# Kernel optimization log

Measured on AMD Instinct MI355X. Metric: run time of the kernel, lower is better.

Reference implementation:

```python
import jax, jax.numpy as jnp
import numpy as np

DIM = 768
HEADS = 12
HEAD_DIM = DIM // HEADS
SCALE = float(HEAD_DIM) ** 0.5  # original multiplies by sqrt(head_dim) (qk_scale=None)


def setup_inputs() -> dict:
    key = jax.random.key(0)
    ks = jax.random.split(key, 6)
    B, N, C = 4, 2048, DIM
    x = jax.random.normal(ks[0], (B, N, C), dtype=jnp.float32)
    qkv_w = jax.random.normal(ks[1], (3 * C, C), dtype=jnp.float32) * (C ** -0.5)
    proj_w = jax.random.normal(ks[2], (C, C), dtype=jnp.float32) * (C ** -0.5)
    proj_b = jnp.zeros((C,), dtype=jnp.float32)
    ln_gamma = jnp.ones((C,), dtype=jnp.float32)
    ln_beta = jnp.zeros((C,), dtype=jnp.float32)
    return {"x": x, "qkv_w": qkv_w, "proj_w": proj_w, "proj_b": proj_b,
            "ln_gamma": ln_gamma, "ln_beta": ln_beta}


def reference(x, qkv_w, proj_w, proj_b, ln_gamma, ln_beta):
    B, N, C = x.shape
    H, D = HEADS, HEAD_DIM
    # qkv: Linear(dim, 3*dim, bias=False) -> reshape (B,N,3,H,D) -> permute to (3,B,H,N,D)
    qkv = jnp.einsum('bnc,oc->bno', x, qkv_w).reshape(B, N, 3, H, D)
    qkv = jnp.transpose(qkv, (2, 0, 3, 1, 4))  # [3,B,H,N,D]
    q, k, v = qkv[0], qkv[1], qkv[2]
    # explicit N x N attention (faithful to the hand-coded matmul path)
    attn = jnp.einsum('bhnd,bhmd->bhnm', q, k) * SCALE
    attn = jax.nn.softmax(attn, axis=-1)
    # dropout is identity at inference
    x1 = jnp.einsum('bhnm,bhmd->bhnd', attn, v)
    x1 = jnp.transpose(x1, (0, 2, 1, 3)).reshape(B, N, C)
    x1 = jnp.einsum('bnc,oc->bno', x1, proj_w) + proj_b
    out = x + x1
    # LayerNorm over last dim (eps = 1e-5, torch default)
    mu = jnp.mean(out, axis=-1, keepdims=True)
    var = jnp.var(out, axis=-1, keepdims=True)
    out = (out - mu) * jax.lax.rsqrt(var + 1e-5) * ln_gamma + ln_beta
    return out
```

## Files before the change

kernel.cpp:

```cpp
#include <hip/hip_runtime.h>

typedef unsigned short u16;
typedef __attribute__((ext_vector_type(8))) short bf16x8;
typedef __attribute__((ext_vector_type(8))) _Float16 f16x8;
typedef __attribute__((ext_vector_type(4))) float f32x4;
typedef __attribute__((ext_vector_type(4))) unsigned short us4;
typedef __attribute__((ext_vector_type(4))) unsigned int u32x4;

#define DEV static __device__ __forceinline__

DEV u16 bf_rne(float x){
    unsigned int u = __builtin_bit_cast(unsigned int, x);
    return (u16)((u + 0x7fffu + ((u >> 16) & 1u)) >> 16);
}
DEV u16 f16_rne(float x){ _Float16 h = (_Float16)x; return __builtin_bit_cast(unsigned short, h); }
DEV unsigned int cvtpk_bf16(float a, float b){
    unsigned int r;
    asm("v_cvt_pk_bf16_f32 %0, %1, %2" : "=v"(r) : "v"(a), "v"(b));
    return r;
}
DEV float exp2_fast(float x){
    float r;
    asm("v_exp_f32 %0, %1" : "=v"(r) : "v"(x));
    return r;
}
DEV void gload_lds16(const void* g, void* l){
    __builtin_amdgcn_global_load_lds((const __attribute__((address_space(1))) unsigned int*)g,
                                     (__attribute__((address_space(3))) unsigned int*)l, 16, 0, 0);
}

#define QSCALE 11.541560327111707f
#define DEFER_THR 11.0f

#define SW(r,cb) ((((cb) ^ ((r)&7)))*8)

__global__ __launch_bounds__(256) void k_prep(const float4* __restrict__ x, const float4* __restrict__ w,
                                              const float4* __restrict__ pw,
                                              u16* __restrict__ xh, u16* __restrict__ xl,
                                              u16* __restrict__ wf, u16* __restrict__ pwh){
    int i = blockIdx.x*256 + threadIdx.x;
    if (i < 1572864){
        float4 v = x[i];
        float vv[4] = {v.x, v.y, v.z, v.w};
        us4 h, l;
        #pragma unroll
        for (int j = 0; j < 4; ++j){
            _Float16 hh = (_Float16)vv[j];
            h[j] = __builtin_bit_cast(unsigned short, hh);
            _Float16 ll = (_Float16)(vv[j] - (float)hh);
            l[j] = __builtin_bit_cast(unsigned short, ll);
        }
        ((us4*)xh)[i] = h;
        ((us4*)xl)[i] = l;
    } else if (i < 1572864 + 442368){
        int j = i - 1572864;
        float4 v = w[j];
        us4 h = { f16_rne(v.x), f16_rne(v.y), f16_rne(v.z), f16_rne(v.w) };
        ((us4*)wf)[j] = h;
    } else {
        int j = i - 2015232;
        float4 v = pw[j];
        us4 h = { bf_rne(v.x), bf_rne(v.y), bf_rne(v.z), bf_rne(v.w) };
        ((us4*)pwh)[j] = h;
    }
}

__global__ __launch_bounds__(256, 3) void k_qkv(const u16* __restrict__ xh_, const u16* __restrict__ xl_,
                                                const u16* __restrict__ wf_,
                                                u16* __restrict__ qf, u16* __restrict__ kf,
                                                u16* __restrict__ vt){
    __shared__ u16 Ah[128*64], Al[128*64], Bf[128*64];
    const int tid = threadIdx.x, lane = tid & 63, wid = tid >> 6;
    const int lm = lane & 15, lg = lane >> 4;
    const int n0 = blockIdx.x * 128, m0 = blockIdx.y * 128;
    const int t = n0 / 768;
    const bool is_v = (t == 2);
    const int wm = (wid >> 1) * 64, wn = (wid & 1) * 64;
    f32x4 acc[4][4];
    const f32x4 z = {0.f, 0.f, 0.f, 0.f};
    #pragma unroll
    for (int i = 0; i < 4; ++i) for (int j = 0; j < 4; ++j) acc[i][j] = z;

    const int c0 = tid;
    for (int kp = 0; kp < 12; ++kp){
        const int kb = kp * 64;
        #pragma unroll
        for (int i = 0; i < 4; ++i){
            int c = c0 + i*256;
            int r = c >> 3, j = c & 7;
            int sj = (j ^ (r & 7)) * 8;
            gload_lds16(xh_ + (size_t)(m0+r)*768 + kb + sj, Ah + c*8);
            if (!is_v)
                gload_lds16(xl_ + (size_t)(m0+r)*768 + kb + sj, Al + c*8);
            gload_lds16(wf_ + (size_t)(n0+r)*768 + kb + sj, Bf + c*8);
        }
        __syncthreads();
        #pragma unroll
        for (int ks = 0; ks < 2; ++ks){
            f16x8 a_h[4], a_l[4], b_f[4];
            #pragma unroll
            for (int mt = 0; mt < 4; ++mt){
                int r = wm + mt*16 + lm, cb = lg + 4*ks;
                a_h[mt] = *(const f16x8*)(Ah + r*64 + SW(r,cb));
                if (!is_v) a_l[mt] = *(const f16x8*)(Al + r*64 + SW(r,cb));
            }
            #pragma unroll
            for (int nt = 0; nt < 4; ++nt){
                int r = wn + nt*16 + lm, cb = lg + 4*ks;
                b_f[nt] = *(const f16x8*)(Bf + r*64 + SW(r,cb));
            }
            #pragma unroll
            for (int mt = 0; mt < 4; ++mt)
            #pragma unroll
            for (int nt = 0; nt < 4; ++nt){
                acc[mt][nt] = __builtin_amdgcn_mfma_f32_16x16x32_f16(a_h[mt], b_f[nt], acc[mt][nt], 0,0,0);
                if (!is_v)
                    acc[mt][nt] = __builtin_amdgcn_mfma_f32_16x16x32_f16(a_l[mt], b_f[nt], acc[mt][nt], 0,0,0);
            }
        }
        __syncthreads();
    }
    const int nb = n0 % 768;
    #pragma unroll
    for (int mt = 0; mt < 4; ++mt)
    #pragma unroll
    for (int nt = 0; nt < 4; ++nt)
    #pragma unroll
    for (int rr = 0; rr < 4; ++rr){
        int grow = m0 + wm + mt*16 + lg*4 + rr;
        int dcol = wn + nt*16 + lm;
        int b = grow >> 11, n = grow & 2047;
        int head = (nb + dcol) >> 6;
        int d    = (nb + dcol) & 63;
        float v = acc[mt][nt][rr];
        if (t == 0)      qf[((size_t)((b*12 + head)*2048 + n))*64 + d] = f16_rne(v * QSCALE);
        else if (t == 1) kf[((size_t)((b*12 + head)*2048 + n))*64 + d] = f16_rne(v);
        else             vt[((size_t)((b*12 + head)*64 + d))*2048 + n] = bf_rne(v);
    }
}

__global__ __launch_bounds__(256) void k_attn(const u16* __restrict__ qf, const u16* __restrict__ kf,
                                              const u16* __restrict__ vt, u16* __restrict__ x1h){
    __shared__ u16 Kf[2][64*64], Vs[2][64*64];
    const int tid = threadIdx.x, lane = tid & 63, wid = tid >> 6;
    const int lm = lane & 15, lg = lane >> 4;
    const size_t bh_base = (size_t)blockIdx.y * 2048 * 64;
    const int q0 = blockIdx.x * 64;

    f16x8 qb[2];
    {
        const u16* qp = qf + bh_base + (size_t)(q0 + wid*16 + lm)*64;
        qb[0] = *(const f16x8*)(qp + lg*8);
        qb[1] = *(const f16x8*)(qp + lg*8 + 32);
    }
    f32x4 o_acc[4];
    const f32x4 z = {0.f,0.f,0.f,0.f};
    #pragma unroll
    for (int i = 0; i < 4; ++i) o_acc[i] = z;
    float m_run = -INFINITY, l_run = 0.f;

    const int srcA = ((lg & 1) * 2) * 16 + lm;
    const int srcB = srcA + 16;
    const int hi_sel = lg >> 1;

    const int r0 = tid >> 3, cb0 = tid & 7;
    const int dK0 = r0*64 + SW(r0,cb0),      dK1 = (r0+32)*64 + SW(r0+32,cb0);
    const u16* kbase = kf + bh_base + r0*64 + cb0*8;
    const u16* vbase = vt + bh_base + (size_t)r0*2048 + cb0*8;

    bf16x8 sK0, sK1, sV0, sV1;
    sK0 = *(const bf16x8*)(kbase);
    sK1 = *(const bf16x8*)(kbase + 2048);
    sV0 = *(const bf16x8*)(vbase);
    sV1 = *(const bf16x8*)(vbase + 32*2048);
    *(bf16x8*)(Kf[0] + dK0) = sK0;  *(bf16x8*)(Kf[0] + dK1) = sK1;
    *(bf16x8*)(Vs[0] + dK0) = sV0;  *(bf16x8*)(Vs[0] + dK1) = sV1;
    __syncthreads();

    for (int kt = 0; kt < 32; ++kt){
        const int cur = kt & 1;
        if (kt < 31){
            const u16* kp = kbase + (kt+1)*4096;
            const u16* vp = vbase + (kt+1)*64;
            sK0 = *(const bf16x8*)(kp);
            sK1 = *(const bf16x8*)(kp + 2048);
            sV0 = *(const bf16x8*)(vp);
            sV1 = *(const bf16x8*)(vp + 32*2048);
        }
        const u16* Kc = Kf[cur];
        const u16* Vc = Vs[cur];
        f32x4 st[4];
        #pragma unroll
        for (int i = 0; i < 4; ++i) st[i] = z;
        #pragma unroll
        for (int ks = 0; ks < 2; ++ks){
            #pragma unroll
            for (int nt = 0; nt < 4; ++nt){
                int r = nt*16 + lm, cb = lg + 4*ks;
                f16x8 ka = *(const f16x8*)(Kc + r*64 + SW(r,cb));
                st[nt] = __builtin_amdgcn_mfma_f32_16x16x32_f16(ka, qb[ks], st[nt], 0,0,0);
            }
        }
        float mx0 = fmaxf(fmaxf(st[0][0], st[0][1]), fmaxf(st[0][2], st[0][3]));
        float mx1 = fmaxf(fmaxf(st[1][0], st[1][1]), fmaxf(st[1][2], st[1][3]));
        float mx2 = fmaxf(fmaxf(st[2][0], st[2][1]), fmaxf(st[2][2], st[2][3]));
        float mx3 = fmaxf(fmaxf(st[3][0], st[3][1]), fmaxf(st[3][2], st[3][3]));
        float lmax = fmaxf(fmaxf(mx0, mx1), fmaxf(mx2, mx3));
        lmax = fmaxf(lmax, __shfl_xor(lmax, 16, 64));
        lmax = fmaxf(lmax, __shfl_xor(lmax, 32, 64));
        if (__any(lmax > m_run + DEFER_THR)){
            float mnew = fmaxf(m_run, lmax);
            float corr = exp2_fast(m_run - mnew);
            m_run = mnew;
            l_run *= corr;
            #pragma unroll
            for (int rr = 0; rr < 4; ++rr){
                float cq = __shfl(corr, (lane & 48) | (lg*4 + rr), 64);
                #pragma unroll
                for (int dt = 0; dt < 4; ++dt) o_acc[dt][rr] *= cq;
            }
        }
        float p[16];
        #pragma unroll
        for (int nt = 0; nt < 4; ++nt)
        #pragma unroll
        for (int rr = 0; rr < 4; ++rr)
            p[nt*4+rr] = exp2_fast(st[nt][rr] - m_run);
        float s01 = (p[0]+p[1]) + (p[2]+p[3]);
        float s23 = (p[4]+p[5]) + (p[6]+p[7]);
        float s45 = (p[8]+p[9]) + (p[10]+p[11]);
        float s67 = (p[12]+p[13]) + (p[14]+p[15]);
        float rsum = (s01+s23) + (s45+s67);
        rsum += __shfl_xor(rsum, 16, 64);
        rsum += __shfl_xor(rsum, 32, 64);
        l_run += rsum;
        unsigned int pk[4][2];
        #pragma unroll
        for (int nt = 0; nt < 4; ++nt)
        #pragma unroll
        for (int h = 0; h < 2; ++h)
            pk[nt][h] = cvtpk_bf16(p[nt*4 + 2*h], p[nt*4 + 2*h + 1]);
        #pragma unroll
        for (int ks = 0; ks < 2; ++ks){
            unsigned int w0a = __shfl(pk[ks*2][0],   srcA, 64);
            unsigned int w0b = __shfl(pk[ks*2+1][0], srcA, 64);
            unsigned int w1a = __shfl(pk[ks*2][1],   srcA, 64);
            unsigned int w1b = __shfl(pk[ks*2+1][1], srcA, 64);
            unsigned int w2a = __shfl(pk[ks*2][0],   srcB, 64);
            unsigned int w2b = __shfl(pk[ks*2+1][0], srcB, 64);
            unsigned int w3a = __shfl(pk[ks*2][1],   srcB, 64);
            unsigned int w3b = __shfl(pk[ks*2+1][1], srcB, 64);
            u32x4 wv;
            wv[0] = hi_sel ? w0b : w0a;
            wv[1] = hi_sel ? w1b : w1a;
            wv[2] = hi_sel ? w2b : w2a;
            wv[3] = hi_sel ? w3b : w3a;
            bf16x8 pa = __builtin_bit_cast(bf16x8, wv);
            #pragma unroll
            for (int dt = 0; dt < 4; ++dt){
                int r = dt*16 + lm, cb = lg + 4*ks;
                bf16x8 vb = *(const bf16x8*)(Vc + r*64 + SW(r,cb));
                o_acc[dt] = __builtin_amdgcn_mfma_f32_16x16x32_bf16(pa, vb, o_acc[dt], 0,0,0);
            }
        }
        __syncthreads();
        if (kt < 31){
            u16* Kn = Kf[cur ^ 1];
            u16* Vn = Vs[cur ^ 1];
            *(bf16x8*)(Kn + dK0) = sK0;  *(bf16x8*)(Kn + dK1) = sK1;
            *(bf16x8*)(Vn + dK0) = sV0;  *(bf16x8*)(Vn + dK1) = sV1;
        }
        __syncthreads();
    }
    const int b = blockIdx.y / 12, hh = blockIdx.y % 12;
    #pragma unroll
    for (int rr = 0; rr < 4; ++rr){
        float lr = __shfl(l_run, (lane & 48) | (lg*4 + rr), 64);
        float linv = 1.0f / lr;
        int qrow = q0 + wid*16 + lg*4 + rr;
        #pragma unroll
        for (int dt = 0; dt < 4; ++dt){
            int cc = hh*64 + dt*16 + lm;
            x1h[((size_t)(b*2048 + qrow))*768 + cc] = bf_rne(o_acc[dt][rr] * linv);
        }
    }
}

__global__ __launch_bounds__(256) void k_proj(const u16* __restrict__ x1h, const u16* __restrict__ pwh,
                                              const float* __restrict__ pb, const float* __restrict__ xres,
                                              float* __restrict__ out){
    __shared__ u16 Ah[128*64], Bh[64*64];
    const int tid = threadIdx.x, lane = tid & 63, wid = tid >> 6;
    const int lm = lane & 15, lg = lane >> 4;
    const int n0 = blockIdx.x * 64, m0 = blockIdx.y * 128;
    const int wm = (wid >> 1) * 64, wn = (wid & 1) * 32;
    f32x4 acc[4][2];
    const f32x4 z = {0.f,0.f,0.f,0.f};
    #pragma unroll
    for (int i = 0; i < 4; ++i) for (int j = 0; j < 2; ++j) acc[i][j] = z;

    for (int kp = 0; kp < 12; ++kp){
        const int kb = kp * 64;
        #pragma unroll
        for (int c = tid; c < 1024; c += 256){
            int r = c >> 3, cb = c & 7;
            *(bf16x8*)(Ah + r*64 + SW(r,cb)) = *(const bf16x8*)(x1h + (size_t)(m0+r)*768 + kb + cb*8);
        }
        #pragma unroll
        for (int c = tid; c < 512; c += 256){
            int r = c >> 3, cb = c & 7;
            *(bf16x8*)(Bh + r*64 + SW(r,cb)) = *(const bf16x8*)(pwh + (size_t)(n0+r)*768 + kb + cb*8);
        }
        __syncthreads();
        #pragma unroll
        for (int ks = 0; ks < 2; ++ks){
            bf16x8 af[4], bfr[2];
            #pragma unroll
            for (int mt = 0; mt < 4; ++mt){
                int r = wm + mt*16 + lm, cb = lg + 4*ks;
                af[mt] = *(const bf16x8*)(Ah + r*64 + SW(r,cb));
            }
            #pragma unroll
            for (int nt = 0; nt < 2; ++nt){
                int r = wn + nt*16 + lm, cb = lg + 4*ks;
                bfr[nt] = *(const bf16x8*)(Bh + r*64 + SW(r,cb));
            }
            #pragma unroll
            for (int mt = 0; mt < 4; ++mt)
            #pragma unroll
            for (int nt = 0; nt < 2; ++nt)
                acc[mt][nt] = __builtin_amdgcn_mfma_f32_16x16x32_bf16(af[mt], bfr[nt], acc[mt][nt], 0,0,0);
        }
        __syncthreads();
    }
    #pragma unroll
    for (int mt = 0; mt < 4; ++mt)
    #pragma unroll
    for (int nt = 0; nt < 2; ++nt)
    #pragma unroll
    for (int rr = 0; rr < 4; ++rr){
        int grow = m0 + wm + mt*16 + lg*4 + rr;
        int gcol = n0 + wn + nt*16 + lm;
        size_t o = (size_t)grow*768 + gcol;
        out[o] = acc[mt][nt][rr] + pb[gcol] + xres[o];
    }
}

__global__ __launch_bounds__(256) void k_ln(float* __restrict__ out, const float* __restrict__ gamma,
                                            const float* __restrict__ beta){
    const int tid = threadIdx.x, lane = tid & 63, wid = tid >> 6;
    float* p = out + (size_t)blockIdx.x * 768;
    float v[3], s = 0.f, s2 = 0.f;
    #pragma unroll
    for (int j = 0; j < 3; ++j){ v[j] = p[tid + j*256]; s += v[j]; s2 += v[j]*v[j]; }
    #pragma unroll
    for (int mm = 1; mm < 64; mm <<= 1){ s += __shfl_xor(s, mm, 64); s2 += __shfl_xor(s2, mm, 64); }
    __shared__ float red[8];
    if (lane == 0){ red[wid] = s; red[4 + wid] = s2; }
    __syncthreads();
    s  = red[0] + red[1] + red[2] + red[3];
    s2 = red[4] + red[5] + red[6] + red[7];
    const float mu  = s * (1.0f/768.0f);
    const float var = s2 * (1.0f/768.0f) - mu*mu;
    const float inv = rsqrtf(var + 1e-5f);
    #pragma unroll
    for (int j = 0; j < 3; ++j){
        int c = tid + j*256;
        p[c] = (v[j] - mu) * inv * gamma[c] + beta[c];
    }
}

extern "C" void kernel_launch(void* const* d_in, const int* in_sizes, int n_in,
                              void* d_out, int out_size, void* d_ws, size_t ws_size,
                              hipStream_t stream){
    const float* x      = (const float*)d_in[0];
    const float* qkv_w  = (const float*)d_in[1];
    const float* proj_w = (const float*)d_in[2];
    const float* pb     = (const float*)d_in[3];
    const float* gamma  = (const float*)d_in[4];
    const float* beta   = (const float*)d_in[5];
    float* out = (float*)d_out;

    constexpr size_t SZ_X   = 8192ull * 768;
    constexpr size_t SZ_W   = 2304ull * 768;
    constexpr size_t SZ_PW  = 768ull * 768;
    constexpr size_t TOTAL  = 6*SZ_X + SZ_W + SZ_PW;
    if (ws_size < TOTAL * sizeof(u16)) return;

    u16* ws  = (u16*)d_ws;
    u16* xh  = ws;
    u16* xl  = xh  + SZ_X;
    u16* wf  = xl  + SZ_X;
    u16* pwh = wf  + SZ_W;
    u16* qf  = pwh + SZ_PW;
    u16* kf  = qf  + SZ_X;
    u16* vt  = kf  + SZ_X;
    u16* x1h = vt  + SZ_X;

    k_prep<<<8448, 256, 0, stream>>>((const float4*)x, (const float4*)qkv_w, (const float4*)proj_w,
                                     xh, xl, wf, pwh);
    k_qkv <<<dim3(18, 64), 256, 0, stream>>>(xh, xl, wf, qf, kf, vt);
    k_attn<<<dim3(32, 48), 256, 0, stream>>>(qf, kf, vt, x1h);
    k_proj<<<dim3(12, 64), 256, 0, stream>>>(x1h, pwh, pb, x, out);
    k_ln  <<<8192, 256, 0, stream>>>(out, gamma, beta);
}
```

Baseline: 330.3 us.

## Drop split-f16 x in QKV GEMM, async LDS staging and MFMA row sums in attention

The QKV GEMM stops using the hi/lo f16 split of x and does a single f16 MFMA per tile. That removes one LDS buffer and half the MFMAs, and occupancy is raised to 4 blocks. The attention kernel now stages K/V with direct global-to-LDS loads instead of register round-trips, which removes one barrier per iteration. It also computes softmax row sums with an extra MFMA against a ones vector instead of shuffle reductions, and uses v_max3 for the row max. Dropping the low part lowers the precision of Q/K, which the scaled logits may amplify.

```diff
diff --git a/kernel.cpp b/kernel.cpp
--- a/kernel.cpp
+++ b/kernel.cpp
@@ -24,6 +24,11 @@
     asm("v_exp_f32 %0, %1" : "=v"(r) : "v"(x));
     return r;
 }
+DEV float max3f(float a, float b, float c){
+    float r;
+    asm("v_max3_f32 %0, %1, %2, %3" : "=v"(r) : "v"(a), "v"(b), "v"(c));
+    return r;
+}
 DEV void gload_lds16(const void* g, void* l){
     __builtin_amdgcn_global_load_lds((const __attribute__((address_space(1))) unsigned int*)g,
                                      (__attribute__((address_space(3))) unsigned int*)l, 16, 0, 0);
@@ -36,22 +41,13 @@
 
 __global__ __launch_bounds__(256) void k_prep(const float4* __restrict__ x, const float4* __restrict__ w,
                                               const float4* __restrict__ pw,
-                                              u16* __restrict__ xh, u16* __restrict__ xl,
-                                              u16* __restrict__ wf, u16* __restrict__ pwh){
+                                              u16* __restrict__ xf, u16* __restrict__ wf,
+                                              u16* __restrict__ pwh){
     int i = blockIdx.x*256 + threadIdx.x;
     if (i < 1572864){
         float4 v = x[i];
-        float vv[4] = {v.x, v.y, v.z, v.w};
-        us4 h, l;
-        #pragma unroll
-        for (int j = 0; j < 4; ++j){
-            _Float16 hh = (_Float16)vv[j];
-            h[j] = __builtin_bit_cast(unsigned short, hh);
-            _Float16 ll = (_Float16)(vv[j] - (float)hh);
-            l[j] = __builtin_bit_cast(unsigned short, ll);
-        }
-        ((us4*)xh)[i] = h;
-        ((us4*)xl)[i] = l;
+        us4 h = { f16_rne(v.x), f16_rne(v.y), f16_rne(v.z), f16_rne(v.w) };
+        ((us4*)xf)[i] = h;
     } else if (i < 1572864 + 442368){
         int j = i - 1572864;
         float4 v = w[j];
@@ -65,44 +61,40 @@
     }
 }
 
-__global__ __launch_bounds__(256, 3) void k_qkv(const u16* __restrict__ xh_, const u16* __restrict__ xl_,
-                                                const u16* __restrict__ wf_,
+__global__ __launch_bounds__(256, 4) void k_qkv(const u16* __restrict__ xf_, const u16* __restrict__ wf_,
                                                 u16* __restrict__ qf, u16* __restrict__ kf,
                                                 u16* __restrict__ vt){
-    __shared__ u16 Ah[128*64], Al[128*64], Bf[128*64];
+    __shared__ u16 Ah[128*64], Bf[128*64];
     const int tid = threadIdx.x, lane = tid & 63, wid = tid >> 6;
     const int lm = lane & 15, lg = lane >> 4;
     const int n0 = blockIdx.x * 128, m0 = blockIdx.y * 128;
     const int t = n0 / 768;
-    const bool is_v = (t == 2);
     const int wm = (wid >> 1) * 64, wn = (wid & 1) * 64;
     f32x4 acc[4][4];
     const f32x4 z = {0.f, 0.f, 0.f, 0.f};
     #pragma unroll
     for (int i = 0; i < 4; ++i) for (int j = 0; j < 4; ++j) acc[i][j] = z;
 
-    const int c0 = tid;
+    const int rA = tid >> 3, jA = tid & 7;
+    const int sj = (jA ^ (rA & 7)) * 8;
+    const u16* asrc = xf_ + (size_t)(m0 + rA)*768 + sj;
+    const u16* bsrc = wf_ + (size_t)(n0 + rA)*768 + sj;
+
     for (int kp = 0; kp < 12; ++kp){
         const int kb = kp * 64;
         #pragma unroll
         for (int i = 0; i < 4; ++i){
-            int c = c0 + i*256;
-            int r = c >> 3, j = c & 7;
-            int sj = (j ^ (r & 7)) * 8;
-            gload_lds16(xh_ + (size_t)(m0+r)*768 + kb + sj, Ah + c*8);
-            if (!is_v)
-                gload_lds16(xl_ + (size_t)(m0+r)*768 + kb + sj, Al + c*8);
-            gload_lds16(wf_ + (size_t)(n0+r)*768 + kb + sj, Bf + c*8);
+            gload_lds16(asrc + (size_t)i*(32*768) + kb, Ah + tid*8 + i*2048);
+            gload_lds16(bsrc + (size_t)i*(32*768) + kb, Bf + tid*8 + i*2048);
         }
         __syncthreads();
         #pragma unroll
         for (int ks = 0; ks < 2; ++ks){
-            f16x8 a_h[4], a_l[4], b_f[4];
+            f16x8 a_f[4], b_f[4];
             #pragma unroll
             for (int mt = 0; mt < 4; ++mt){
                 int r = wm + mt*16 + lm, cb = lg + 4*ks;
-                a_h[mt] = *(const f16x8*)(Ah + r*64 + SW(r,cb));
-                if (!is_v) a_l[mt] = *(const f16x8*)(Al + r*64 + SW(r,cb));
+                a_f[mt] = *(const f16x8*)(Ah + r*64 + SW(r,cb));
             }
             #pragma unroll
             for (int nt = 0; nt < 4; ++nt){
@@ -112,11 +104,8 @@
             #pragma unroll
             for (int mt = 0; mt < 4; ++mt)
             #pragma unroll
-            for (int nt = 0; nt < 4; ++nt){
-                acc[mt][nt] = __builtin_amdgcn_mfma_f32_16x16x32_f16(a_h[mt], b_f[nt], acc[mt][nt], 0,0,0);
-                if (!is_v)
-                    acc[mt][nt] = __builtin_amdgcn_mfma_f32_16x16x32_f16(a_l[mt], b_f[nt], acc[mt][nt], 0,0,0);
-            }
+            for (int nt = 0; nt < 4; ++nt)
+                acc[mt][nt] = __builtin_amdgcn_mfma_f32_16x16x32_f16(a_f[mt], b_f[nt], acc[mt][nt], 0,0,0);
         }
         __syncthreads();
     }
@@ -153,40 +142,42 @@
         qb[0] = *(const f16x8*)(qp + lg*8);
         qb[1] = *(const f16x8*)(qp + lg*8 + 32);
     }
-    f32x4 o_acc[4];
+    f32x4 o_acc[4], o_sum;
     const f32x4 z = {0.f,0.f,0.f,0.f};
     #pragma unroll
     for (int i = 0; i < 4; ++i) o_acc[i] = z;
-    float m_run = -INFINITY, l_run = 0.f;
+    o_sum = z;
+    float m_run = -INFINITY;
+    bf16x8 ones;
+    #pragma unroll
+    for (int i = 0; i < 8; ++i) ones[i] = (short)16256;
 
     const int srcA = ((lg & 1) * 2) * 16 + lm;
     const int srcB = srcA + 16;
     const int hi_sel = lg >> 1;
 
-    const int r0 = tid >> 3, cb0 = tid & 7;
-    const int dK0 = r0*64 + SW(r0,cb0),      dK1 = (r0+32)*64 + SW(r0+32,cb0);
-    const u16* kbase = kf + bh_base + r0*64 + cb0*8;
-    const u16* vbase = vt + bh_base + (size_t)r0*2048 + cb0*8;
-
-    bf16x8 sK0, sK1, sV0, sV1;
-    sK0 = *(const bf16x8*)(kbase);
-    sK1 = *(const bf16x8*)(kbase + 2048);
-    sV0 = *(const bf16x8*)(vbase);
-    sV1 = *(const bf16x8*)(vbase + 32*2048);
-    *(bf16x8*)(Kf[0] + dK0) = sK0;  *(bf16x8*)(Kf[0] + dK1) = sK1;
-    *(bf16x8*)(Vs[0] + dK0) = sV0;  *(bf16x8*)(Vs[0] + dK1) = sV1;
+    const int rA = tid >> 3, jA = tid & 7;
+    const int sj = (jA ^ (rA & 7)) * 8;
+    const u16* ksrc = kf + bh_base + rA*64 + sj;
+    const u16* vsrc = vt + bh_base + (size_t)rA*2048 + sj;
+
+    #define STAGE(kt_, b_) do { \
+        const u16* kp_ = ksrc + (size_t)(kt_)*4096; \
+        const u16* vp_ = vsrc + (size_t)(kt_)*64; \
+        u16* lk_ = Kf[b_] + tid*8; \
+        u16* lv_ = Vs[b_] + tid*8; \
+        gload_lds16(kp_,            lk_); \
+        gload_lds16(kp_ + 2048,     lk_ + 2048); \
+        gload_lds16(vp_,            lv_); \
+        gload_lds16(vp_ + 32*2048,  lv_ + 2048); \
+    } while(0)
+
+    STAGE(0, 0);
     __syncthreads();
 
     for (int kt = 0; kt < 32; ++kt){
         const int cur = kt & 1;
-        if (kt < 31){
-            const u16* kp = kbase + (kt+1)*4096;
-            const u16* vp = vbase + (kt+1)*64;
-            sK0 = *(const bf16x8*)(kp);
-            sK1 = *(const bf16x8*)(kp + 2048);
-            sV0 = *(const bf16x8*)(vp);
-            sV1 = *(const bf16x8*)(vp + 32*2048);
-        }
+        if (kt < 31) STAGE(kt + 1, cur ^ 1);
         const u16* Kc = Kf[cur];
         const u16* Vc = Vs[cur];
         f32x4 st[4];
@@ -201,21 +192,22 @@
                 st[nt] = __builtin_amdgcn_mfma_f32_16x16x32_f16(ka, qb[ks], st[nt], 0,0,0);
             }
         }
-        float mx0 = fmaxf(fmaxf(st[0][0], st[0][1]), fmaxf(st[0][2], st[0][3]));
-        float mx1 = fmaxf(fmaxf(st[1][0], st[1][1]), fmaxf(st[1][2], st[1][3]));
-        float mx2 = fmaxf(fmaxf(st[2][0], st[2][1]), fmaxf(st[2][2], st[2][3]));
-        float mx3 = fmaxf(fmaxf(st[3][0], st[3][1]), fmaxf(st[3][2], st[3][3]));
-        float lmax = fmaxf(fmaxf(mx0, mx1), fmaxf(mx2, mx3));
+        float g0 = max3f(st[0][0], st[0][1], st[0][2]);
+        float g1 = max3f(st[0][3], st[1][0], st[1][1]);
+        float g2 = max3f(st[1][2], st[1][3], st[2][0]);
+        float g3 = max3f(st[2][1], st[2][2], st[2][3]);
+        float g4 = max3f(st[3][0], st[3][1], st[3][2]);
+        float lmax = fmaxf(max3f(g0, g1, g2), max3f(g3, g4, st[3][3]));
         lmax = fmaxf(lmax, __shfl_xor(lmax, 16, 64));
         lmax = fmaxf(lmax, __shfl_xor(lmax, 32, 64));
         if (__any(lmax > m_run + DEFER_THR)){
             float mnew = fmaxf(m_run, lmax);
             float corr = exp2_fast(m_run - mnew);
             m_run = mnew;
-            l_run *= corr;
             #pragma unroll
             for (int rr = 0; rr < 4; ++rr){
                 float cq = __shfl(corr, (lane & 48) | (lg*4 + rr), 64);
+                o_sum[rr] *= cq;
                 #pragma unroll
                 for (int dt = 0; dt < 4; ++dt) o_acc[dt][rr] *= cq;
             }
@@ -226,14 +218,6 @@
         #pragma unroll
         for (int rr = 0; rr < 4; ++rr)
             p[nt*4+rr] = exp2_fast(st[nt][rr] - m_run);
-        float s01 = (p[0]+p[1]) + (p[2]+p[3]);
-        float s23 = (p[4]+p[5]) + (p[6]+p[7]);
-        float s45 = (p[8]+p[9]) + (p[10]+p[11]);
-        float s67 = (p[12]+p[13]) + (p[14]+p[15]);
-        float rsum = (s01+s23) + (s45+s67);
-        rsum += __shfl_xor(rsum, 16, 64);
-        rsum += __shfl_xor(rsum, 32, 64);
-        l_run += rsum;
         unsigned int pk[4][2];
         #pragma unroll
         for (int nt = 0; nt < 4; ++nt)
@@ -256,6 +240,7 @@
             wv[2] = hi_sel ? w2b : w2a;
             wv[3] = hi_sel ? w3b : w3a;
             bf16x8 pa = __builtin_bit_cast(bf16x8, wv);
+            o_sum = __builtin_amdgcn_mfma_f32_16x16x32_bf16(pa, ones, o_sum, 0,0,0);
             #pragma unroll
             for (int dt = 0; dt < 4; ++dt){
                 int r = dt*16 + lm, cb = lg + 4*ks;
@@ -264,19 +249,12 @@
             }
         }
         __syncthreads();
-        if (kt < 31){
-            u16* Kn = Kf[cur ^ 1];
-            u16* Vn = Vs[cur ^ 1];
-            *(bf16x8*)(Kn + dK0) = sK0;  *(bf16x8*)(Kn + dK1) = sK1;
-            *(bf16x8*)(Vn + dK0) = sV0;  *(bf16x8*)(Vn + dK1) = sV1;
-        }
-        __syncthreads();
-    }
+    }
+    #undef STAGE
     const int b = blockIdx.y / 12, hh = blockIdx.y % 12;
     #pragma unroll
     for (int rr = 0; rr < 4; ++rr){
-        float lr = __shfl(l_run, (lane & 48) | (lg*4 + rr), 64);
-        float linv = 1.0f / lr;
+        float linv = 1.0f / o_sum[rr];
         int qrow = q0 + wid*16 + lg*4 + rr;
         #pragma unroll
         for (int dt = 0; dt < 4; ++dt){
@@ -384,13 +362,12 @@
     constexpr size_t SZ_X   = 8192ull * 768;
     constexpr size_t SZ_W   = 2304ull * 768;
     constexpr size_t SZ_PW  = 768ull * 768;
-    constexpr size_t TOTAL  = 6*SZ_X + SZ_W + SZ_PW;
+    constexpr size_t TOTAL  = 5*SZ_X + SZ_W + SZ_PW;
     if (ws_size < TOTAL * sizeof(u16)) return;
 
     u16* ws  = (u16*)d_ws;
-    u16* xh  = ws;
-    u16* xl  = xh  + SZ_X;
-    u16* wf  = xl  + SZ_X;
+    u16* xf  = ws;
+    u16* wf  = xf  + SZ_X;
     u16* pwh = wf  + SZ_W;
     u16* qf  = pwh + SZ_PW;
     u16* kf  = qf  + SZ_X;
@@ -398,8 +375,8 @@
     u16* x1h = vt  + SZ_X;
 
     k_prep<<<8448, 256, 0, stream>>>((const float4*)x, (const float4*)qkv_w, (const float4*)proj_w,
-                                     xh, xl, wf, pwh);
-    k_qkv <<<dim3(18, 64), 256, 0, stream>>>(xh, xl, wf, qf, kf, vt);
+                                     xf, wf, pwh);
+    k_qkv <<<dim3(18, 64), 256, 0, stream>>>(xf, wf, qf, kf, vt);
     k_attn<<<dim3(32, 48), 256, 0, stream>>>(qf, kf, vt, x1h);
     k_proj<<<dim3(12, 64), 256, 0, stream>>>(x1h, pwh, pb, x, out);
     k_ln  <<<8192, 256, 0, stream>>>(out, gamma, beta);
```

New measurement: 326.2 us. About the same (-1.2%).
